# Optimization experiments

Hardware: AMD Instinct MI355X
Metric: run time of the kernel (lower is better)

## Reference

```python
import jax, jax.numpy as jnp
import numpy as np

N_NODES = 100000
N_EDGES = 1_600_000
IN_C, HID_C, CLS_C = 128, 256, 64


def setup_inputs() -> dict:
    key = jax.random.key(0)
    ks = jax.random.split(key, 8)
    x = jax.random.normal(ks[0], (N_NODES, IN_C), dtype=jnp.float32)
    edge_index = jax.random.randint(ks[1], (2, N_EDGES), 0, N_NODES, dtype=jnp.int64)
    s1 = 1.0 / np.sqrt(IN_C)
    s2 = 1.0 / np.sqrt(HID_C)
    W1l = jax.random.uniform(ks[2], (IN_C, HID_C), jnp.float32, -s1, s1)
    W1r = jax.random.uniform(ks[3], (IN_C, HID_C), jnp.float32, -s1, s1)
    b1 = jnp.zeros((HID_C,), jnp.float32)
    W2l = jax.random.uniform(ks[4], (HID_C, CLS_C), jnp.float32, -s2, s2)
    W2r = jax.random.uniform(ks[5], (HID_C, CLS_C), jnp.float32, -s2, s2)
    b2 = jnp.zeros((CLS_C,), jnp.float32)
    return {"x": x, "edge_index": edge_index,
            "W1l": W1l, "W1r": W1r, "b1": b1,
            "W2l": W2l, "W2r": W2r, "b2": b2}


def _sage_conv(x, src, dst, Wl, Wr, b, num_nodes):
    # mean aggregation of source features onto destination nodes
    agg = jax.ops.segment_sum(x[src], dst, num_segments=num_nodes)  # [N, F]
    deg = jax.ops.segment_sum(jnp.ones((src.shape[0], 1), x.dtype), dst,
                              num_segments=num_nodes)               # [N, 1]
    agg = agg / jnp.maximum(deg, 1.0)  # zero-degree nodes -> 0
    return agg @ Wl + x @ Wr + b


def reference(x, edge_index, W1l, W1r, b1, W2l, W2r, b2):
    src, dst = edge_index[0], edge_index[1]
    n = x.shape[0]
    h = jax.nn.relu(_sage_conv(x, src, dst, W1l, W1r, b1, n))
    # dropout(p=0.5) is identity in eval mode
    out = _sage_conv(h, src, dst, W2l, W2r, b2, n)
    return jax.nn.sigmoid(out)
```

## Files before the change

kernel.cpp:

```cpp
#include <hip/hip_runtime.h>

typedef __attribute__((ext_vector_type(8))) short short8;
typedef __attribute__((ext_vector_type(4))) float floatx4;
typedef __attribute__((ext_vector_type(2))) float floatx2;

static __device__ __forceinline__ unsigned short f2bf(float f) {
  unsigned int u = __builtin_bit_cast(unsigned int, f);
  u += 0x7FFFu + ((u >> 16) & 1u);
  return (unsigned short)(u >> 16);
}
static __device__ __forceinline__ float bf2f(unsigned short s) {
  unsigned int u = ((unsigned int)s) << 16;
  return __builtin_bit_cast(float, u);
}
static __device__ __forceinline__ unsigned int pk4_fp8(float a, float b, float c, float d) {
  int lo = __builtin_amdgcn_cvt_pk_fp8_f32(a, b, 0, false);
  int hi = __builtin_amdgcn_cvt_pk_fp8_f32(c, d, 0, false);
  return (unsigned int)((lo & 0xffff) | ((hi & 0xffff) << 16));
}
static __device__ __forceinline__ floatx4 unpk4_fp8(unsigned int p) {
  floatx2 lo = __builtin_amdgcn_cvt_pk_f32_fp8((int)p, false);
  floatx2 hi = __builtin_amdgcn_cvt_pk_f32_fp8((int)p, true);
  floatx4 r = {lo.x, lo.y, hi.x, hi.y};
  return r;
}

#define NBUCK 2048
#define BIN_CHUNK 8192
#define ECAP 1536


__global__ __launch_bounds__(256) void bhist(const int* __restrict__ dst,
                                             int* __restrict__ bcnt, int E) {
  __shared__ int h[NBUCK];
  for (int i = threadIdx.x; i < NBUCK; i += 256) h[i] = 0;
  __syncthreads();
  int stride = gridDim.x * 256;
  for (int i = blockIdx.x * 256 + threadIdx.x; i < E; i += stride)
    atomicAdd(&h[dst[i] >> 6], 1);
  __syncthreads();
  for (int i = threadIdx.x; i < NBUCK; i += 256)
    if (h[i]) atomicAdd(&bcnt[i], h[i]);
}

__global__ __launch_bounds__(256) void bscan(const int* __restrict__ bcnt,
                                             int* __restrict__ bbase,
                                             int* __restrict__ bcur,
                                             int* __restrict__ rs, int N, int E) {
  __shared__ int ps[256];
  int t = threadIdx.x;
  int v[8]; int tsum = 0;
#pragma unroll
  for (int j = 0; j < 8; j++) { v[j] = bcnt[t * 8 + j]; tsum += v[j]; }
  ps[t] = tsum;
  __syncthreads();
  for (int off = 1; off < 256; off <<= 1) {
    int xx = (t >= off) ? ps[t - off] : 0;
    __syncthreads();
    ps[t] += xx;
    __syncthreads();
  }
  int run = ps[t] - tsum;
#pragma unroll
  for (int j = 0; j < 8; j++) {
    bbase[t * 8 + j] = run; bcur[t * 8 + j] = run; run += v[j];
  }
  if (t == 0) rs[N] = E;
}

__global__ __launch_bounds__(256) void binscatter(const int* __restrict__ src,
                                                  const int* __restrict__ dst,
                                                  int* __restrict__ bcur,
                                                  unsigned int* __restrict__ staging,
                                                  int E) {
  __shared__ int h[NBUCK];
  __shared__ int cur[NBUCK];
  for (int i = threadIdx.x; i < NBUCK; i += 256) h[i] = 0;
  __syncthreads();
  int base = blockIdx.x * BIN_CHUNK;
  int end = base + BIN_CHUNK; if (end > E) end = E;
  for (int i = base + threadIdx.x; i < end; i += 256)
    atomicAdd(&h[dst[i] >> 6], 1);
  __syncthreads();
  for (int i = threadIdx.x; i < NBUCK; i += 256)
    cur[i] = h[i] ? atomicAdd(&bcur[i], h[i]) : 0;
  __syncthreads();
  for (int i = base + threadIdx.x; i < end; i += 256) {
    int d = dst[i], s = src[i];
    int b = d >> 6;
    int pos = atomicAdd(&cur[b], 1);
    staging[pos] = ((unsigned int)(d & 63) << 17) | (unsigned int)s;
  }
}

__global__ void convw(const float* __restrict__ W1l, const float* __restrict__ W1r,
                      const float* __restrict__ W2l, const float* __restrict__ W2r,
                      unsigned short* __restrict__ W1p, unsigned short* __restrict__ W2p) {
  int i = blockIdx.x * blockDim.x + threadIdx.x;
  if (i < 8192) {
    int lane = i & 63, ni = (i >> 6) & 1, kk = (i >> 7) & 7, w = i >> 10;
    int fm = lane & 15, fq = lane >> 4;
    int n = w * 32 + ni * 16 + fm;
    int k0 = kk * 32 + fq * 8;
    unsigned short r[8];
#pragma unroll
    for (int j = 0; j < 8; j++) {
      int k = k0 + j;
      float v = (k < 128) ? W1l[k * 256 + n] : W1r[(k - 128) * 256 + n];
      r[j] = f2bf(v);
    }
    *reinterpret_cast<uint4*>(W1p + (size_t)i * 8) = *reinterpret_cast<uint4*>(r);
  } else if (i < 8192 + 4096) {
    int j2 = i - 8192;
    int lane = j2 & 63, kk = (j2 >> 6) & 7, w = j2 >> 9;
    int fm = lane & 15, fq = lane >> 4;
    int n = w * 16 + fm;
    int k0 = kk * 32 + fq * 8;
    unsigned short r[8];
#pragma unroll
    for (int j = 0; j < 8; j++) {
      int k = k0 + j;
      float v = (n < 64) ? W2l[k * 64 + n] : W2r[k * 64 + (n - 64)];
      r[j] = f2bf(v);
    }
    *reinterpret_cast<uint4*>(W2p + (size_t)j2 * 8) = *reinterpret_cast<uint4*>(r);
  }
}

__global__ void convx(const float* __restrict__ x, unsigned int* __restrict__ xq,
                      int n_nodes) {
  int i = blockIdx.x * blockDim.x + threadIdx.x;
  if (i < n_nodes * 32) {
    int node = i >> 5, c4 = (i & 31) * 4;
    float4 v = *reinterpret_cast<const float4*>(x + (size_t)node * 128 + c4);
    xq[i] = pk4_fp8(v.x, v.y, v.z, v.w);
  }
}

#define LDSW 264
__global__ __launch_bounds__(512, 6) void gemm_fused(const float* __restrict__ x,
                                                     const uint4* __restrict__ xq,
                                                     const unsigned int* __restrict__ staging,
                                                     const int* __restrict__ bbase,
                                                     const int* __restrict__ bcnt,
                                                     const unsigned short* __restrict__ W1p,
                                                     const unsigned short* __restrict__ W2p,
                                                     const float* __restrict__ b1,
                                                     unsigned char* __restrict__ zq,
                                                     unsigned short* __restrict__ rb,
                                                     int* __restrict__ csr_src,
                                                     int* __restrict__ rs,
                                                     int M) {
  __shared__ unsigned short smem[64 * LDSW];
  __shared__ int eidx[ECAP];
  __shared__ int h64[64], rstart[64], cur64[64];
  const int tid = threadIdx.x;
  const int lane = tid & 63;
  const int wave = tid >> 6;
  const int m0 = blockIdx.x * 64;
  const int fm = lane & 15;
  const int fq = lane >> 4;
  const int base = bbase[blockIdx.x];
  const int cnt = bcnt[blockIdx.x];
  const short8* __restrict__ W1v = reinterpret_cast<const short8*>(W1p);
  const short8* __restrict__ W2v = reinterpret_cast<const short8*>(W2p);

  if (tid < 64) h64[tid] = 0;
  __syncthreads();

#pragma unroll
  for (int j = 0; j < 4; j++) {
    int c = j * 512 + tid;
    int row = c >> 5, f4 = c & 31;
    int gr = m0 + row; if (gr >= M) gr = M - 1;
    float4 v = *reinterpret_cast<const float4*>(x + (size_t)gr * 128 + f4 * 4);
    unsigned short r[4] = { f2bf(v.x), f2bf(v.y), f2bf(v.z), f2bf(v.w) };
    *reinterpret_cast<uint2*>(&smem[row * LDSW + 128 + f4 * 4]) =
        *reinterpret_cast<uint2*>(r);
  }

  for (int i = tid; i < cnt; i += 512)
    atomicAdd(&h64[staging[base + i] >> 17], 1);
  __syncthreads();

  if (tid < 64) {
    int v = h64[tid];
    int s = v;
#pragma unroll
    for (int off = 1; off < 64; off <<= 1) {
      int o = __shfl_up(s, off, 64);
      if (tid >= off) s += o;
    }
    int excl = s - v;
    rstart[tid] = excl;
    cur64[tid] = excl;
    int w = m0 + tid;
    if (w < M) rs[w] = base + excl;
  }
  __syncthreads();

  for (int i = tid; i < cnt; i += 512) {
    unsigned int wv = staging[base + i];
    int pos = atomicAdd(&cur64[wv >> 17], 1);
    if (pos < ECAP) eidx[pos] = (int)(wv & 0x1FFFFu);
  }
  __syncthreads();

  for (int i = tid; i < cnt && i < ECAP; i += 512)
    csr_src[base + i] = eidx[i];

  {
    const int grp = lane >> 3;
    const int ch4 = lane & 7;
    int row = wave * 8 + grp;
    int e0l = rstart[row];
    int e1l = e0l + h64[row];
    if (e1l > ECAP) e1l = ECAP;
    floatx4 a0[4] = {{0,0,0,0},{0,0,0,0},{0,0,0,0},{0,0,0,0}};
    floatx4 a1[4] = {{0,0,0,0},{0,0,0,0},{0,0,0,0},{0,0,0,0}};
    for (int e = e0l; e < e1l; e += 8) {
      uint4 pb[8];
#pragma unroll
      for (int j = 0; j < 8; j++) {
        int t = e + j; if (t >= e1l) t = e1l - 1;
        int s = eidx[t];
        pb[j] = xq[(s << 3) | ch4];
      }
      int rem = e1l - e;
#pragma unroll
      for (int j = 0; j < 8; j++) {
        if (j < rem) {
          floatx4* acc = (j & 1) ? a1 : a0;
          acc[0] += unpk4_fp8(pb[j].x);
          acc[1] += unpk4_fp8(pb[j].y);
          acc[2] += unpk4_fp8(pb[j].z);
          acc[3] += unpk4_fp8(pb[j].w);
        }
      }
    }
    int d = e1l - e0l; if (d < 1) d = 1;
    float sc = 1.0f / (float)d;
    unsigned short r[16];
#pragma unroll
    for (int j = 0; j < 4; j++) {
      floatx4 a = a0[j] + a1[j];
      r[4 * j + 0] = f2bf(a.x * sc); r[4 * j + 1] = f2bf(a.y * sc);
      r[4 * j + 2] = f2bf(a.z * sc); r[4 * j + 3] = f2bf(a.w * sc);
    }
    unsigned short* dstp = &smem[row * LDSW + ch4 * 16];
    *reinterpret_cast<uint4*>(dstp) = *reinterpret_cast<uint4*>(r);
    *reinterpret_cast<uint4*>(dstp + 8) = *reinterpret_cast<uint4*>(r + 8);
  }

  float bb[2];
#pragma unroll
  for (int ni = 0; ni < 2; ni++) bb[ni] = b1[wave * 32 + ni * 16 + fm];

  __syncthreads();

  floatx4 acc1[4][2] = {};
#pragma unroll 2
  for (int kk = 0; kk < 8; kk++) {
    short8 af[4], bfr[2];
#pragma unroll
    for (int mi = 0; mi < 4; mi++)
      af[mi] = *reinterpret_cast<const short8*>(
          &smem[(mi * 16 + fm) * LDSW + kk * 32 + fq * 8]);
#pragma unroll
    for (int ni = 0; ni < 2; ni++)
      bfr[ni] = W1v[((wave * 8 + kk) * 2 + ni) * 64 + lane];
#pragma unroll
    for (int mi = 0; mi < 4; mi++)
#pragma unroll
      for (int ni = 0; ni < 2; ni++)
        acc1[mi][ni] = __builtin_amdgcn_mfma_f32_16x16x32_bf16(af[mi], bfr[ni],
                                                               acc1[mi][ni], 0, 0, 0);
  }

  __syncthreads();

#pragma unroll
  for (int mi = 0; mi < 4; mi++)
#pragma unroll
    for (int ni = 0; ni < 2; ni++)
#pragma unroll
      for (int r = 0; r < 4; r++) {
        float v = acc1[mi][ni][r] + bb[ni];
        v = v > 0.f ? v : 0.f;
        smem[(mi * 16 + fq * 4 + r) * LDSW + wave * 32 + ni * 16 + fm] = f2bf(v);
      }
  __syncthreads();

  floatx4 acc2[4] = {};
#pragma unroll 2
  for (int kk = 0; kk < 8; kk++) {
    short8 hf[4];
#pragma unroll
    for (int mi = 0; mi < 4; mi++)
      hf[mi] = *reinterpret_cast<const short8*>(
          &smem[(mi * 16 + fm) * LDSW + kk * 32 + fq * 8]);
    short8 wf = W2v[(wave * 8 + kk) * 64 + lane];
#pragma unroll
    for (int mi = 0; mi < 4; mi++)
      acc2[mi] = __builtin_amdgcn_mfma_f32_16x16x32_bf16(hf[mi], wf, acc2[mi], 0, 0, 0);
  }

#pragma unroll
  for (int mi = 0; mi < 4; mi++)
#pragma unroll
    for (int r = 0; r < 4; r++) {
      int grow = m0 + mi * 16 + fq * 4 + r;
      if (grow < M) {
        float v = acc2[mi][r];
        if (wave < 4) {
          int col = wave * 16 + fm;
          int b8 = __builtin_amdgcn_cvt_pk_fp8_f32(v, v, 0, false);
          zq[grow * 64 + col] = (unsigned char)(b8 & 0xff);
        } else {
          int col = (wave - 4) * 16 + fm;
          rb[grow * 64 + col] = f2bf(v);
        }
      }
    }
}

__global__ __launch_bounds__(256) void agg2_final(const uint4* __restrict__ zq,
                                                  const unsigned short* __restrict__ rb,
                                                  const int* __restrict__ csr_src,
                                                  const int* __restrict__ rs,
                                                  const float* __restrict__ b2,
                                                  float* __restrict__ out, int n_nodes) {
  int lane = threadIdx.x & 63;
  int wave = threadIdx.x >> 6;
  int grp = lane >> 2;
  int ch = lane & 3;
  int lbase = lane & 60;
  int w = blockIdx.x * 64 + wave * 16 + grp;
  if (w >= n_nodes) return;
  int e0 = rs[w], e1 = rs[w + 1];
  floatx4 a0[4] = {{0,0,0,0},{0,0,0,0},{0,0,0,0},{0,0,0,0}};
  floatx4 a1[4] = {{0,0,0,0},{0,0,0,0},{0,0,0,0},{0,0,0,0}};
  for (int e = e0; e < e1; e += 8) {
    int tA = e + ch;     if (tA >= e1) tA = e1 - 1;
    int tB = e + 4 + ch; if (tB >= e1) tB = e1 - 1;
    int iA = csr_src[tA];
    int iB = csr_src[tB];
    uint4 pb[8];
#pragma unroll
    for (int j = 0; j < 4; j++) {
      int s = __shfl(iA, lbase | j, 64);
      pb[j] = zq[(s << 2) | ch];
    }
#pragma unroll
    for (int j = 0; j < 4; j++) {
      int s = __shfl(iB, lbase | j, 64);
      pb[4 + j] = zq[(s << 2) | ch];
    }
    int rem = e1 - e;
#pragma unroll
    for (int j = 0; j < 8; j++) {
      if (j < rem) {
        floatx4* acc = (j & 1) ? a1 : a0;
        acc[0] += unpk4_fp8(pb[j].x);
        acc[1] += unpk4_fp8(pb[j].y);
        acc[2] += unpk4_fp8(pb[j].z);
        acc[3] += unpk4_fp8(pb[j].w);
      }
    }
  }
  int d = e1 - e0; if (d < 1) d = 1;
  float sc = 1.0f / (float)d;
  const unsigned short* rbp = rb + w * 64 + ch * 16;
  const float* b2p = b2 + ch * 16;
  float* op = out + (size_t)w * 64 + ch * 16;
#pragma unroll
  for (int j = 0; j < 4; j++) {
    floatx4 a = a0[j] + a1[j];
    uint2 rr = *reinterpret_cast<const uint2*>(rbp + 4 * j);
    float4 bv = *reinterpret_cast<const float4*>(b2p + 4 * j);
    float r0 = bf2f((unsigned short)(rr.x & 0xffff));
    float r1 = bf2f((unsigned short)(rr.x >> 16));
    float r2 = bf2f((unsigned short)(rr.y & 0xffff));
    float r3 = bf2f((unsigned short)(rr.y >> 16));
    float4 o;
    o.x = 1.0f / (1.0f + __expf(-(a.x * sc + r0 + bv.x)));
    o.y = 1.0f / (1.0f + __expf(-(a.y * sc + r1 + bv.y)));
    o.z = 1.0f / (1.0f + __expf(-(a.z * sc + r2 + bv.z)));
    o.w = 1.0f / (1.0f + __expf(-(a.w * sc + r3 + bv.w)));
    *reinterpret_cast<float4*>(op + 4 * j) = o;
  }
}

extern "C" void kernel_launch(void* const* d_in, const int* in_sizes, int n_in,
                              void* d_out, int out_size, void* d_ws, size_t ws_size,
                              hipStream_t stream) {
  const float* x   = (const float*)d_in[0];
  const int*   ei  = (const int*)d_in[1];
  const float* W1l = (const float*)d_in[2];
  const float* W1r = (const float*)d_in[3];
  const float* b1  = (const float*)d_in[4];
  const float* W2l = (const float*)d_in[5];
  const float* W2r = (const float*)d_in[6];
  const float* b2  = (const float*)d_in[7];
  float* out = (float*)d_out;

  const int N = in_sizes[0] / 128;
  const int E = in_sizes[1] / 2;
  const int* src = ei;
  const int* dst = ei + E;

  char* wsb = (char*)d_ws;
  size_t off = 0;
  auto alloc = [&](size_t bytes) -> void* {
    void* p = wsb + off;
    off += (bytes + 511) & ~(size_t)511;
    return p;
  };
  int* rs       = (int*)alloc((size_t)(N + 1) * 4);
  int* csr_src  = (int*)alloc((size_t)E * 4 + 64);
  int* bcnt     = (int*)alloc(NBUCK * 4);
  int* bbase    = (int*)alloc(NBUCK * 4);
  int* bcur     = (int*)alloc(NBUCK * 4);
  unsigned int* staging = (unsigned int*)alloc((size_t)E * 4);
  unsigned short* W1p = (unsigned short*)alloc(256 * 256 * 2);
  unsigned short* W2p = (unsigned short*)alloc(128 * 256 * 2);
  unsigned int* xq    = (unsigned int*)alloc((size_t)N * 128);
  unsigned char* zq   = (unsigned char*)alloc((size_t)N * 64);
  unsigned short* rb  = (unsigned short*)alloc((size_t)N * 64 * 2);
  (void)ws_size; (void)n_in; (void)out_size;

  const int ntiles = (N + 63) / 64;
  const int nchunks = (E + BIN_CHUNK - 1) / BIN_CHUNK;

  hipMemsetAsync(bcnt, 0, NBUCK * 4, stream);
  bhist<<<256, 256, 0, stream>>>(dst, bcnt, E);
  bscan<<<1, 256, 0, stream>>>(bcnt, bbase, bcur, rs, N, E);
  binscatter<<<nchunks, 256, 0, stream>>>(src, dst, bcur, staging, E);

  convw<<<(8192 + 4096 + 255) / 256, 256, 0, stream>>>(W1l, W1r, W2l, W2r, W1p, W2p);
  convx<<<(N * 32 + 255) / 256, 256, 0, stream>>>(x, xq, N);

  gemm_fused<<<ntiles, 512, 0, stream>>>(x, (const uint4*)xq, staging, bbase, bcnt,
                                         W1p, W2p, b1, zq, rb, csr_src, rs, N);

  agg2_final<<<(N + 63) / 64, 256, 0, stream>>>((const uint4*)zq, rb, csr_src, rs, b2, out, N);
}
```

Baseline: 238.8 us.

## Replace histogram+scan with fixed-capacity per-bucket staging and precompute bf16 x

Drops the global histogram and scan kernels by giving each 64-node bucket a fixed SCAP-slot region in staging and csr_src, with bcnt used directly as the per-bucket cursor. Row ends become rs plus an explicit deg array instead of rs[w+1]. convx now also writes a bf16 copy of x, so gemm_fused loads bf16 directly instead of converting fp32 in the tile. This removes two launches and a pass over dst, but silently drops edges beyond SCAP per bucket (average is about 1024) and adds an extra N*128*2 byte write and read of bf16 x.

```diff
diff --git a/kernel.cpp b/kernel.cpp
--- a/kernel.cpp
+++ b/kernel.cpp
@@ -27,50 +27,11 @@
 
 #define NBUCK 2048
 #define BIN_CHUNK 8192
-#define ECAP 1536
-
-
-__global__ __launch_bounds__(256) void bhist(const int* __restrict__ dst,
-                                             int* __restrict__ bcnt, int E) {
-  __shared__ int h[NBUCK];
-  for (int i = threadIdx.x; i < NBUCK; i += 256) h[i] = 0;
-  __syncthreads();
-  int stride = gridDim.x * 256;
-  for (int i = blockIdx.x * 256 + threadIdx.x; i < E; i += stride)
-    atomicAdd(&h[dst[i] >> 6], 1);
-  __syncthreads();
-  for (int i = threadIdx.x; i < NBUCK; i += 256)
-    if (h[i]) atomicAdd(&bcnt[i], h[i]);
-}
-
-__global__ __launch_bounds__(256) void bscan(const int* __restrict__ bcnt,
-                                             int* __restrict__ bbase,
-                                             int* __restrict__ bcur,
-                                             int* __restrict__ rs, int N, int E) {
-  __shared__ int ps[256];
-  int t = threadIdx.x;
-  int v[8]; int tsum = 0;
-#pragma unroll
-  for (int j = 0; j < 8; j++) { v[j] = bcnt[t * 8 + j]; tsum += v[j]; }
-  ps[t] = tsum;
-  __syncthreads();
-  for (int off = 1; off < 256; off <<= 1) {
-    int xx = (t >= off) ? ps[t - off] : 0;
-    __syncthreads();
-    ps[t] += xx;
-    __syncthreads();
-  }
-  int run = ps[t] - tsum;
-#pragma unroll
-  for (int j = 0; j < 8; j++) {
-    bbase[t * 8 + j] = run; bcur[t * 8 + j] = run; run += v[j];
-  }
-  if (t == 0) rs[N] = E;
-}
+#define SCAP 1536
 
 __global__ __launch_bounds__(256) void binscatter(const int* __restrict__ src,
                                                   const int* __restrict__ dst,
-                                                  int* __restrict__ bcur,
+                                                  int* __restrict__ bcnt,
                                                   unsigned int* __restrict__ staging,
                                                   int E) {
   __shared__ int h[NBUCK];
@@ -83,13 +44,14 @@
     atomicAdd(&h[dst[i] >> 6], 1);
   __syncthreads();
   for (int i = threadIdx.x; i < NBUCK; i += 256)
-    cur[i] = h[i] ? atomicAdd(&bcur[i], h[i]) : 0;
+    cur[i] = h[i] ? atomicAdd(&bcnt[i], h[i]) : 0;
   __syncthreads();
   for (int i = base + threadIdx.x; i < end; i += 256) {
     int d = dst[i], s = src[i];
     int b = d >> 6;
     int pos = atomicAdd(&cur[b], 1);
-    staging[pos] = ((unsigned int)(d & 63) << 17) | (unsigned int)s;
+    if (pos < SCAP)
+      staging[(size_t)b * SCAP + pos] = ((unsigned int)(d & 63) << 17) | (unsigned int)s;
   }
 }
 
@@ -128,20 +90,22 @@
 }
 
 __global__ void convx(const float* __restrict__ x, unsigned int* __restrict__ xq,
-                      int n_nodes) {
+                      unsigned short* __restrict__ xbf, int n_nodes) {
   int i = blockIdx.x * blockDim.x + threadIdx.x;
   if (i < n_nodes * 32) {
     int node = i >> 5, c4 = (i & 31) * 4;
     float4 v = *reinterpret_cast<const float4*>(x + (size_t)node * 128 + c4);
     xq[i] = pk4_fp8(v.x, v.y, v.z, v.w);
+    unsigned short r[4] = { f2bf(v.x), f2bf(v.y), f2bf(v.z), f2bf(v.w) };
+    *reinterpret_cast<uint2*>(xbf + (size_t)node * 128 + c4) =
+        *reinterpret_cast<uint2*>(r);
   }
 }
 
 #define LDSW 264
-__global__ __launch_bounds__(512, 6) void gemm_fused(const float* __restrict__ x,
+__global__ __launch_bounds__(512, 6) void gemm_fused(const unsigned short* __restrict__ xbf,
                                                      const uint4* __restrict__ xq,
                                                      const unsigned int* __restrict__ staging,
-                                                     const int* __restrict__ bbase,
                                                      const int* __restrict__ bcnt,
                                                      const unsigned short* __restrict__ W1p,
                                                      const unsigned short* __restrict__ W2p,
@@ -150,9 +114,10 @@
                                                      unsigned short* __restrict__ rb,
                                                      int* __restrict__ csr_src,
                                                      int* __restrict__ rs,
+                                                     int* __restrict__ deg,
                                                      int M) {
   __shared__ unsigned short smem[64 * LDSW];
-  __shared__ int eidx[ECAP];
+  __shared__ int eidx[SCAP];
   __shared__ int h64[64], rstart[64], cur64[64];
   const int tid = threadIdx.x;
   const int lane = tid & 63;
@@ -160,8 +125,8 @@
   const int m0 = blockIdx.x * 64;
   const int fm = lane & 15;
   const int fq = lane >> 4;
-  const int base = bbase[blockIdx.x];
-  const int cnt = bcnt[blockIdx.x];
+  const int base = blockIdx.x * SCAP;
+  int cnt = bcnt[blockIdx.x]; if (cnt > SCAP) cnt = SCAP;
   const short8* __restrict__ W1v = reinterpret_cast<const short8*>(W1p);
   const short8* __restrict__ W2v = reinterpret_cast<const short8*>(W2p);
 
@@ -169,14 +134,12 @@
   __syncthreads();
 
 #pragma unroll
-  for (int j = 0; j < 4; j++) {
+  for (int j = 0; j < 2; j++) {
     int c = j * 512 + tid;
-    int row = c >> 5, f4 = c & 31;
+    int row = c >> 4, u4 = c & 15;
     int gr = m0 + row; if (gr >= M) gr = M - 1;
-    float4 v = *reinterpret_cast<const float4*>(x + (size_t)gr * 128 + f4 * 4);
-    unsigned short r[4] = { f2bf(v.x), f2bf(v.y), f2bf(v.z), f2bf(v.w) };
-    *reinterpret_cast<uint2*>(&smem[row * LDSW + 128 + f4 * 4]) =
-        *reinterpret_cast<uint2*>(r);
+    uint4 v = *reinterpret_cast<const uint4*>(xbf + (size_t)gr * 128 + u4 * 8);
+    *reinterpret_cast<uint4*>(&smem[row * LDSW + 128 + u4 * 8]) = v;
   }
 
   for (int i = tid; i < cnt; i += 512)
@@ -195,18 +158,18 @@
     rstart[tid] = excl;
     cur64[tid] = excl;
     int w = m0 + tid;
-    if (w < M) rs[w] = base + excl;
+    if (w < M) { rs[w] = base + excl; deg[w] = v; }
   }
   __syncthreads();
 
   for (int i = tid; i < cnt; i += 512) {
     unsigned int wv = staging[base + i];
     int pos = atomicAdd(&cur64[wv >> 17], 1);
-    if (pos < ECAP) eidx[pos] = (int)(wv & 0x1FFFFu);
-  }
-  __syncthreads();
-
-  for (int i = tid; i < cnt && i < ECAP; i += 512)
+    if (pos < SCAP) eidx[pos] = (int)(wv & 0x1FFFFu);
+  }
+  __syncthreads();
+
+  for (int i = tid; i < cnt; i += 512)
     csr_src[base + i] = eidx[i];
 
   {
@@ -215,7 +178,7 @@
     int row = wave * 8 + grp;
     int e0l = rstart[row];
     int e1l = e0l + h64[row];
-    if (e1l > ECAP) e1l = ECAP;
+    if (e1l > SCAP) e1l = SCAP;
     floatx4 a0[4] = {{0,0,0,0},{0,0,0,0},{0,0,0,0},{0,0,0,0}};
     floatx4 a1[4] = {{0,0,0,0},{0,0,0,0},{0,0,0,0},{0,0,0,0}};
     for (int e = e0l; e < e1l; e += 8) {
@@ -328,6 +291,7 @@
                                                   const unsigned short* __restrict__ rb,
                                                   const int* __restrict__ csr_src,
                                                   const int* __restrict__ rs,
+                                                  const int* __restrict__ deg,
                                                   const float* __restrict__ b2,
                                                   float* __restrict__ out, int n_nodes) {
   int lane = threadIdx.x & 63;
@@ -337,7 +301,7 @@
   int lbase = lane & 60;
   int w = blockIdx.x * 64 + wave * 16 + grp;
   if (w >= n_nodes) return;
-  int e0 = rs[w], e1 = rs[w + 1];
+  int e0 = rs[w], e1 = e0 + deg[w];
   floatx4 a0[4] = {{0,0,0,0},{0,0,0,0},{0,0,0,0},{0,0,0,0}};
   floatx4 a1[4] = {{0,0,0,0},{0,0,0,0},{0,0,0,0},{0,0,0,0}};
   for (int e = e0; e < e1; e += 8) {
@@ -416,15 +380,15 @@
     off += (bytes + 511) & ~(size_t)511;
     return p;
   };
-  int* rs       = (int*)alloc((size_t)(N + 1) * 4);
-  int* csr_src  = (int*)alloc((size_t)E * 4 + 64);
+  int* rs       = (int*)alloc((size_t)N * 4);
+  int* deg      = (int*)alloc((size_t)N * 4);
   int* bcnt     = (int*)alloc(NBUCK * 4);
-  int* bbase    = (int*)alloc(NBUCK * 4);
-  int* bcur     = (int*)alloc(NBUCK * 4);
-  unsigned int* staging = (unsigned int*)alloc((size_t)E * 4);
+  int* csr_src  = (int*)alloc((size_t)NBUCK * SCAP * 4);
+  unsigned int* staging = (unsigned int*)alloc((size_t)NBUCK * SCAP * 4);
   unsigned short* W1p = (unsigned short*)alloc(256 * 256 * 2);
   unsigned short* W2p = (unsigned short*)alloc(128 * 256 * 2);
   unsigned int* xq    = (unsigned int*)alloc((size_t)N * 128);
+  unsigned short* xbf = (unsigned short*)alloc((size_t)N * 128 * 2);
   unsigned char* zq   = (unsigned char*)alloc((size_t)N * 64);
   unsigned short* rb  = (unsigned short*)alloc((size_t)N * 64 * 2);
   (void)ws_size; (void)n_in; (void)out_size;
@@ -433,15 +397,14 @@
   const int nchunks = (E + BIN_CHUNK - 1) / BIN_CHUNK;
 
   hipMemsetAsync(bcnt, 0, NBUCK * 4, stream);
-  bhist<<<256, 256, 0, stream>>>(dst, bcnt, E);
-  bscan<<<1, 256, 0, stream>>>(bcnt, bbase, bcur, rs, N, E);
-  binscatter<<<nchunks, 256, 0, stream>>>(src, dst, bcur, staging, E);
+  binscatter<<<nchunks, 256, 0, stream>>>(src, dst, bcnt, staging, E);
 
   convw<<<(8192 + 4096 + 255) / 256, 256, 0, stream>>>(W1l, W1r, W2l, W2r, W1p, W2p);
-  convx<<<(N * 32 + 255) / 256, 256, 0, stream>>>(x, xq, N);
-
-  gemm_fused<<<ntiles, 512, 0, stream>>>(x, (const uint4*)xq, staging, bbase, bcnt,
-                                         W1p, W2p, b1, zq, rb, csr_src, rs, N);
-
-  agg2_final<<<(N + 63) / 64, 256, 0, stream>>>((const uint4*)zq, rb, csr_src, rs, b2, out, N);
-}
+  convx<<<(N * 32 + 255) / 256, 256, 0, stream>>>(x, xq, xbf, N);
+
+  gemm_fused<<<ntiles, 512, 0, stream>>>(xbf, (const uint4*)xq, staging, bcnt,
+                                         W1p, W2p, b1, zq, rb, csr_src, rs, deg, N);
+
+  agg2_final<<<(N + 63) / 64, 256, 0, stream>>>((const uint4*)zq, rb, csr_src, rs, deg,
+                                                b2, out, N);
+}
```

After: 235.6 us. No clear change (-1.4%).
